# Performance work log

Measured on AMD Instinct MI355X. Metric: run time of the kernel, lower is better.

## Reference

```python
import jax, jax.numpy as jnp
from jax import lax
import numpy as np

D_MODEL = 1024
D_STATE = 16
D_CONV = 4
EXPAND = 2
D_INNER = EXPAND * D_MODEL  # 2048
BATCH = 4
SEQLEN = 2048


def setup_inputs() -> dict:
    key = jax.random.key(0)
    ks = jax.random.split(key, 8)
    s = 0.02  # small init scale for stability
    f32 = jnp.float32
    return {
        "x": jax.random.normal(ks[0], (BATCH, SEQLEN, D_MODEL), f32),
        # Linear weights stored as (in, out); torch applies x @ W.T with W (out, in) -- same math.
        "W_in": (jax.random.normal(ks[1], (D_MODEL, 2 * D_INNER), f32) * s),
        "conv_w": (jax.random.normal(ks[2], (D_INNER, 1, D_CONV), f32) * s),  # depthwise (O, I/groups=1, K)
        "conv_b": jnp.zeros((D_INNER,), f32),
        "W_xproj": (jax.random.normal(ks[3], (D_INNER, 2 * D_STATE), f32) * s),
        "W_dt": (jax.random.normal(ks[4], (D_INNER, D_INNER), f32) * s),
        "b_dt": jnp.zeros((D_INNER,), f32),
        "A_log": jnp.log(jax.random.uniform(ks[5], (D_INNER, D_STATE), f32, 1e-4, 1.0)),
        "D_param": jnp.ones((D_INNER,), f32),
        "W_out": (jax.random.normal(ks[6], (D_INNER, D_MODEL), f32) * s),
    }


def _mamba_forward(x, W_in, conv_w, conv_b, W_xproj, W_dt, b_dt, A_log, D_param, W_out):
    Bb, L, _ = x.shape
    # in_proj and split into x-branch and gate z
    xz = x @ W_in                      # (B, L, 2*d_inner)
    xc, z = jnp.split(xz, 2, axis=-1)
    # causal depthwise conv1d: torch pads both sides by d_conv-1 then slices [:L] == left-pad only
    xt = xc.transpose(0, 2, 1)         # (B, d_inner, L)
    xconv = lax.conv_general_dilated(
        xt, conv_w, window_strides=(1,), padding=[(D_CONV - 1, 0)],
        feature_group_count=D_INNER, dimension_numbers=("NCH", "OIH", "NCH"))
    xs = jax.nn.silu(xconv.transpose(0, 2, 1) + conv_b[None, None, :])  # (B, L, d_inner)
    # SSM inputs
    delta = jax.nn.softplus(xs @ W_dt + b_dt)          # (B, L, d_inner)
    Bs, Cs = jnp.split(xs @ W_xproj, 2, axis=-1)       # each (B, L, d_state)
    A = -jnp.exp(A_log)                                 # (d_inner, d_state)

    def step(h, inp):
        dt, bv, cv, xv = inp                            # (B,d_inner),(B,d_state),(B,d_state),(B,d_inner)
        dA = 1.0 + A[None] * dt[..., None]              # Euler discretization (B, d_inner, d_state)
        dB = bv[:, None, :] * (xv * dt)[..., None]
        h = h * dA + dB
        y = jnp.einsum("bds,bs->bd", h, cv) + D_param * xv
        return h, y

    inputs = (delta.transpose(1, 0, 2), Bs.transpose(1, 0, 2),
              Cs.transpose(1, 0, 2), xs.transpose(1, 0, 2))
    h0 = jnp.zeros((Bb, D_INNER, D_STATE), x.dtype)
    _, ys = lax.scan(step, h0, inputs)                  # ys: (L, B, d_inner)
    y = ys.transpose(1, 0, 2) * jax.nn.silu(z)          # gated output
    return y @ W_out                                    # (B, L, d_model)


def reference(x, W_in, conv_w, conv_b, W_xproj, W_dt, b_dt, A_log, D_param, W_out):
    return _mamba_forward(x, W_in, conv_w, conv_b, W_xproj, W_dt, b_dt, A_log, D_param, W_out)
```

## Files before the change

### kernel.cpp

```cpp
#include <hip/hip_runtime.h>

#define AS1 __attribute__((address_space(1)))
#define AS3 __attribute__((address_space(3)))

typedef unsigned short u16;
typedef unsigned int u32;
typedef __attribute__((ext_vector_type(8))) __bf16 bf16x8;
typedef __attribute__((ext_vector_type(8))) unsigned short u16x8;
typedef __attribute__((ext_vector_type(4))) float f32x4;

#define BATCH   4
#define SEQLEN  2048
#define DMODEL  1024
#define DINNER  2048
#define DSTATE  16
#define ROWS    (BATCH * SEQLEN)

__device__ __forceinline__ u16 f2bf(float f) {
  union { float f; unsigned u; } v; v.f = f;
  unsigned u = v.u;
  return (u16)((u + 0x7fffu + ((u >> 16) & 1u)) >> 16);
}
__device__ __forceinline__ float bf2f(u16 s) {
  union { unsigned u; float f; } v; v.u = ((unsigned)s) << 16;
  return v.f;
}
__device__ __forceinline__ float bflo(u32 p) { union { unsigned u; float f; } v; v.u = p << 16; return v.f; }
__device__ __forceinline__ float bfhi(u32 p) { union { unsigned u; float f; } v; v.u = p & 0xffff0000u; return v.f; }

template<int IMM>
__device__ __forceinline__ bf16x8 dsr(unsigned addr) {
  bf16x8 r;
  asm volatile("ds_read_b128 %0, %1 offset:%2" : "=&v"(r) : "v"(addr), "i"(IMM));
  return r;
}
__device__ __forceinline__ unsigned lds_addr(const u16* p) {
  return (unsigned)(size_t)(const AS3 u16*)p;
}

__global__ void cast_f32_bf16(const float* __restrict__ in, u16* __restrict__ out, int n4) {
  int i = blockIdx.x * blockDim.x + threadIdx.x;
  if (i >= n4) return;
  float4 v = ((const float4*)in)[i];
  ushort4 o;
  o.x = f2bf(v.x); o.y = f2bf(v.y); o.z = f2bf(v.z); o.w = f2bf(v.w);
  ((ushort4*)out)[i] = o;
}

__global__ void transpose_cast(const float* __restrict__ in, u16* __restrict__ out, int R, int C) {
  __shared__ float tile[32][33];
  int x  = blockIdx.x * 32 + threadIdx.x;
  int y0 = blockIdx.y * 32;
#pragma unroll
  for (int j = 0; j < 32; j += 8)
    tile[threadIdx.y + j][threadIdx.x] = in[(size_t)(y0 + threadIdx.y + j) * C + x];
  __syncthreads();
  int xo  = blockIdx.y * 32 + threadIdx.x;
  int yo0 = blockIdx.x * 32;
#pragma unroll
  for (int j = 0; j < 32; j += 8)
    out[(size_t)(yo0 + threadIdx.y + j) * R + xo] = f2bf(tile[threadIdx.x][threadIdx.y + j]);
}

template<int EPI, int BN_>
__launch_bounds__(512, 1)
__global__ void gemm8p(const u16* __restrict__ A, const u16* __restrict__ Bt,
                       void* __restrict__ outp, const float* __restrict__ bias,
                       int M, int N, int K, int gn, int rr, int cc) {
  constexpr int NF   = BN_ / 64;
  constexpr int BCH  = BN_ / 64;
  constexpr int ASZ  = 256 * 64;
  constexpr int BSZ  = BN_ * 64;
  constexpr int BUFS = ASZ + BSZ;
  extern __shared__ u16 lds[];

  const int xcd = blockIdx.x & 7, kb = blockIdx.x >> 3;
  const int tpr = gn / cc;
  const int bm  = (xcd / tpr) * rr + kb / cc;
  const int bn  = (xcd % tpr) * cc + kb % cc;

  const int tid  = threadIdx.x;
  const int wave = tid >> 6, lane = tid & 63;
  const int wm = wave >> 2, wn = wave & 3;
  const int llo = lane & 15, lhi = lane >> 4;
  const size_t bm0 = (size_t)bm * 256, bn0 = (size_t)bn * BN_;
  const int NT = K >> 6;

  const u16* gA[4];
#pragma unroll
  for (int ch = 0; ch < 4; ++ch) {
    int row  = ch * 64 + (tid >> 3);
    int scol = ((tid & 7) ^ (row & 7)) << 3;
    gA[ch] = A + (bm0 + row) * (size_t)K + scol;
  }
  const u16* gB[BCH];
#pragma unroll
  for (int ch = 0; ch < BCH; ++ch) {
    int row  = ch * 64 + (tid >> 3);
    int scol = ((tid & 7) ^ (row & 7)) << 3;
    gB[ch] = Bt + (bn0 + row) * (size_t)K + scol;
  }

  unsigned aA[2][2], aB[2][2];
  {
    const unsigned base0 = lds_addr(lds);
    const unsigned rowA = (unsigned)(wm * 128 + llo) * 128u;
    const unsigned rowB = (unsigned)(wn * (NF * 16) + llo) * 128u;
    const unsigned msk = (unsigned)((llo & 7) << 4);
#pragma unroll
    for (int bf = 0; bf < 2; ++bf)
#pragma unroll
      for (int kk = 0; kk < 2; ++kk) {
        unsigned colk = ((unsigned)(kk * 64 + lhi * 16)) ^ msk;
        aA[bf][kk] = base0 + (unsigned)bf * (BUFS * 2) + rowA + colk;
        aB[bf][kk] = base0 + (unsigned)bf * (BUFS * 2) + (ASZ * 2) + rowB + colk;
      }
  }

#define SGA(t, bsel, ch) __builtin_amdgcn_global_load_lds(                       \
    (const AS1 void*)(gA[ch] + ((size_t)(t) << 6)),                              \
    (AS3 void*)(lds + (bsel) * BUFS + (ch) * 4096 + wave * 512), 16, 0, 0)
#define SGB(t, bsel, ch) __builtin_amdgcn_global_load_lds(                       \
    (const AS1 void*)(gB[ch] + ((size_t)(t) << 6)),                              \
    (AS3 void*)(lds + (bsel) * BUFS + ASZ + (ch) * 4096 + wave * 512), 16, 0, 0)

  f32x4 acc[8][NF] = {};
  bf16x8 bfr[2][4];

#define PHASE(BUF, MH, KK, RDB, STG, WC)                                         \
  {                                                                              \
    bf16x8 af[4];                                                                \
    af[0] = dsr<(MH) * 8192 + 0>(aA[BUF][KK]);                                   \
    af[1] = dsr<(MH) * 8192 + 2048>(aA[BUF][KK]);                                \
    af[2] = dsr<(MH) * 8192 + 4096>(aA[BUF][KK]);                                \
    af[3] = dsr<(MH) * 8192 + 6144>(aA[BUF][KK]);                                \
    if (RDB) {                                                                   \
      bfr[KK][0] = dsr<0>(aB[BUF][KK]);                                          \
      bfr[KK][1] = dsr<2048>(aB[BUF][KK]);                                       \
      if (NF == 4) {                                                             \
        bfr[KK][2] = dsr<4096>(aB[BUF][KK]);                                     \
        bfr[KK][3] = dsr<6144>(aB[BUF][KK]);                                     \
      }                                                                          \
    }                                                                            \
    STG;                                                                         \
    asm volatile("s_barrier" ::: "memory");                                      \
    asm volatile("s_waitcnt lgkmcnt(0)" ::: "memory");                           \
    __builtin_amdgcn_sched_barrier(0);                                           \
    __builtin_amdgcn_s_setprio(1);                                               \
    _Pragma("unroll") for (int m = 0; m < 4; ++m)                                \
      _Pragma("unroll") for (int n = 0; n < NF; ++n)                             \
        acc[(MH) * 4 + m][n] = __builtin_amdgcn_mfma_f32_16x16x32_bf16(          \
            af[m], bfr[KK][n], acc[(MH) * 4 + m][n], 0, 0, 0);                   \
    __builtin_amdgcn_s_setprio(0);                                               \
    WC;                                                                          \
    asm volatile("s_barrier" ::: "memory");                                      \
  }

  SGA(0, 0, 0); SGA(0, 0, 2); SGB(0, 0, 0); SGB(0, 0, 1);
  if (BCH == 4) { SGB(0, 0, 2); SGB(0, 0, 3); }
  SGA(0, 0, 1); SGA(0, 0, 3);
  SGA(1, 1, 0); SGA(1, 1, 2); SGB(1, 1, 0); SGB(1, 1, 1);
  asm volatile("s_waitcnt vmcnt(4)" ::: "memory");
  asm volatile("s_barrier" ::: "memory");

  for (int u = 0; u < NT; u += 2) {
    const int v = u + 1;
    PHASE(0, 0, 0, true,
          ({ if (BCH == 4) { SGB(v, 1, 2); SGB(v, 1, 3); } else { SGA(v, 1, 1); SGA(v, 1, 3); } }),
          ((void)0));
    PHASE(0, 0, 1, true,
          ({ if (BCH == 4) { SGA(v, 1, 1); SGA(v, 1, 3); } }),
          ((void)0));
    PHASE(0, 1, 0, false,
          ({ if (u + 2 < NT) { SGA(u + 2, 0, 0); SGA(u + 2, 0, 2); } }),
          ((void)0));
    PHASE(0, 1, 1, false,
          ({ if (u + 2 < NT) { SGB(u + 2, 0, 0); SGB(u + 2, 0, 1); } }),
          ({ if (u + 2 < NT) asm volatile("s_waitcnt vmcnt(4)" ::: "memory");
             else            asm volatile("s_waitcnt vmcnt(0)" ::: "memory"); }));
    PHASE(1, 0, 0, true,
          ({ if (u + 2 < NT) { if (BCH == 4) { SGB(u + 2, 0, 2); SGB(u + 2, 0, 3); }
                               else          { SGA(u + 2, 0, 1); SGA(u + 2, 0, 3); } } }),
          ((void)0));
    PHASE(1, 0, 1, true,
          ({ if (u + 2 < NT && BCH == 4) { SGA(u + 2, 0, 1); SGA(u + 2, 0, 3); } }),
          ((void)0));
    PHASE(1, 1, 0, false,
          ({ if (v + 2 < NT) { SGA(v + 2, 1, 0); SGA(v + 2, 1, 2); } }),
          ((void)0));
    PHASE(1, 1, 1, false,
          ({ if (v + 2 < NT) { SGB(v + 2, 1, 0); SGB(v + 2, 1, 1); } }),
          ({ if (v + 2 < NT) asm volatile("s_waitcnt vmcnt(4)" ::: "memory");
             else            asm volatile("s_waitcnt vmcnt(0)" ::: "memory"); }));
  }
#undef PHASE
#undef SGA
#undef SGB

#pragma unroll
  for (int am = 0; am < 8; ++am) {
    const int mh = am >> 2, m = am & 3;
    const int rowb = (int)bm0 + wm * 128 + mh * 64 + m * 16 + lhi * 4;
#pragma unroll
    for (int n = 0; n < NF; ++n) {
      const int col = (int)bn0 + wn * (16 * NF) + n * 16 + llo;
#pragma unroll
      for (int r = 0; r < 4; ++r) {
        float v = acc[am][n][r];
        size_t idx = (size_t)(rowb + r) * N + col;
        if (EPI == 0) {
          ((u16*)outp)[idx] = f2bf(v);
        } else if (EPI == 1) {
          float xb = v + bias[col];
          float sp = (xb > 20.f) ? xb : log1pf(__expf(xb));
          ((u16*)outp)[idx] = f2bf(sp);
        } else {
          ((float*)outp)[idx] = v;
        }
      }
    }
  }
}

__global__ void conv_silu4(const u16* __restrict__ xz, const float* __restrict__ w,
                           const float* __restrict__ cb, u16* __restrict__ xs, int total4) {
  int idx = blockIdx.x * 256 + threadIdx.x;
  if (idx >= total4) return;
  int d4 = idx & (DINNER / 4 - 1);
  int l  = (idx >> 9) & (SEQLEN - 1);
  int b  = idx >> 20;
  int d  = d4 * 4;
  float4 wv[4];
#pragma unroll
  for (int j = 0; j < 4; ++j) wv[j] = ((const float4*)w)[d + j];
  float4 bias = *(const float4*)(cb + d);
  float acc[4] = { bias.x, bias.y, bias.z, bias.w };
#pragma unroll
  for (int k = 0; k < 4; ++k) {
    int li = l - 3 + k;
    if (li >= 0) {
      ushort4 xv = *(const ushort4*)(xz + (size_t)(b * SEQLEN + li) * (2 * DINNER) + d);
      acc[0] = fmaf((&wv[0].x)[k], bf2f(xv.x), acc[0]);
      acc[1] = fmaf((&wv[1].x)[k], bf2f(xv.y), acc[1]);
      acc[2] = fmaf((&wv[2].x)[k], bf2f(xv.z), acc[2]);
      acc[3] = fmaf((&wv[3].x)[k], bf2f(xv.w), acc[3]);
    }
  }
  ushort4 o;
  o.x = f2bf(acc[0] / (1.f + __expf(-acc[0])));
  o.y = f2bf(acc[1] / (1.f + __expf(-acc[1])));
  o.z = f2bf(acc[2] / (1.f + __expf(-acc[2])));
  o.w = f2bf(acc[3] / (1.f + __expf(-acc[3])));
  *(ushort4*)(xs + (size_t)idx * 4) = o;
}

__global__ void xproj_kernel(const u16* __restrict__ xs, const float* __restrict__ Wx,
                             float* __restrict__ outp) {
  __shared__ float part[256];
  int row = blockIdx.x;
  int tid = threadIdx.x;
  int c = tid & 31, kp = tid >> 5;
  const u16* xr = xs + (size_t)row * DINNER + kp * 256;
  const float* wp = Wx + (size_t)(kp * 256) * 32 + c;
  float acc = 0.f;
#pragma unroll 4
  for (int kk = 0; kk < 32; ++kk) {
    u16x8 xv = *(const u16x8*)(const void*)(xr + kk * 8);
#pragma unroll
    for (int j = 0; j < 8; ++j)
      acc = fmaf(bf2f(xv[j]), wp[(kk * 8 + j) * 32], acc);
  }
  part[tid] = acc;
  __syncthreads();
  if (tid < 32) {
    float s = 0.f;
#pragma unroll
    for (int p = 0; p < 8; ++p) s += part[p * 32 + tid];
    outp[(size_t)row * 32 + tid] = s;
  }
}

#define SC_NC 32
#define SC_CL 64
#define SC_LDS (2 * SC_NC * 16 * 33 * 4)

__launch_bounds__(512, 1)
__global__ void scan_v3(const u16* __restrict__ delta, const u16* __restrict__ xs,
                        const float* __restrict__ xproj, const u16* __restrict__ xz,
                        const float* __restrict__ A_log, const float* __restrict__ Dp,
                        u16* __restrict__ yg) {
  extern __shared__ float smem[];
  float* cP = smem;
  float* cH = smem + SC_NC * 16 * 33;
  const int tid = threadIdx.x;
  const int dl = tid & 15, ck = tid >> 4;
  const int b = blockIdx.x >> 6, dblk = blockIdx.x & 63;
  const int d0 = dblk * 32 + dl * 2;
  const int r0 = b * SEQLEN + ck * SC_CL;

  float A0[DSTATE], A1[DSTATE];
  {
    const f32x4* ap0 = (const f32x4*)(A_log + (size_t)d0 * DSTATE);
    const f32x4* ap1 = (const f32x4*)(A_log + (size_t)(d0 + 1) * DSTATE);
#pragma unroll
    for (int q = 0; q < 4; ++q) {
      f32x4 a0 = ap0[q], a1 = ap1[q];
#pragma unroll
      for (int j = 0; j < 4; ++j) { A0[q * 4 + j] = -__expf(a0[j]); A1[q * 4 + j] = -__expf(a1[j]); }
    }
  }

  const u32* dP = (const u32*)(delta + (size_t)r0 * DINNER + d0);
  const u32* xP = (const u32*)(xs    + (size_t)r0 * DINNER + d0);
  const u32* zP = (const u32*)(xz + (size_t)r0 * (2 * DINNER) + DINNER + d0);
  const float* bP = xproj + (size_t)r0 * 32;
  const int DW = DINNER / 2;
  const int ZW = DINNER;

  float P0[DSTATE], P1[DSTATE], H0[DSTATE], H1[DSTATE];
#pragma unroll
  for (int s = 0; s < DSTATE; ++s) { P0[s] = P1[s] = 1.f; H0[s] = H1[s] = 0.f; }
  {
    u32 dq0 = dP[0], xq0 = xP[0];
    u32 dq1 = dP[DW], xq1 = xP[DW];
    f32x4 Bn[4];
#pragma unroll
    for (int q = 0; q < 4; ++q) Bn[q] = ((const f32x4*)bP)[q];
    for (int l = 0; l < SC_CL; ++l) {
      const u32 dc = dq0, xc = xq0;
      dq0 = dq1; xq0 = xq1;
      if (l + 2 < SC_CL) { dq1 = dP[(l + 2) * DW]; xq1 = xP[(l + 2) * DW]; }
      f32x4 Bc[4] = { Bn[0], Bn[1], Bn[2], Bn[3] };
      if (l + 1 < SC_CL) {
        const f32x4* bn = (const f32x4*)(bP + (l + 1) * 32);
#pragma unroll
        for (int q = 0; q < 4; ++q) Bn[q] = bn[q];
      }
      float dt0 = bflo(dc), dt1 = bfhi(dc);
      float x0 = bflo(xc),  x1 = bfhi(xc);
      float dtx0 = dt0 * x0, dtx1 = dt1 * x1;
#pragma unroll
      for (int s = 0; s < DSTATE; ++s) {
        float bs = Bc[s >> 2][s & 3];
        float dA0 = fmaf(A0[s], dt0, 1.f);
        float dA1 = fmaf(A1[s], dt1, 1.f);
        P0[s] *= dA0; P1[s] *= dA1;
        H0[s] = fmaf(H0[s], dA0, bs * dtx0);
        H1[s] = fmaf(H1[s], dA1, bs * dtx1);
      }
    }
  }
  {
    float* p = cP + (ck * 16 + dl) * 33;
    float* h = cH + (ck * 16 + dl) * 33;
#pragma unroll
    for (int s = 0; s < DSTATE; ++s) {
      p[s] = P0[s]; p[16 + s] = P1[s];
      h[s] = H0[s]; h[16 + s] = H1[s];
    }
  }
  __syncthreads();

  {
    const int s2 = tid & 15, dd = tid >> 4;
    const int idx = (dd & 1) * 16 + s2;
    float* pbase = cP + (dd >> 1) * 33 + idx;
    float* hbase = cH + (dd >> 1) * 33 + idx;
    float h = 0.f;
    for (int c = 0; c < SC_NC; ++c) {
      float p = pbase[c * 16 * 33], hh = hbase[c * 16 * 33];
      pbase[c * 16 * 33] = h;
      h = fmaf(p, h, hh);
    }
  }
  __syncthreads();

  float h0[DSTATE], h1[DSTATE];
  {
    const float* p = cP + (ck * 16 + dl) * 33;
#pragma unroll
    for (int s = 0; s < DSTATE; ++s) { h0[s] = p[s]; h1[s] = p[16 + s]; }
  }
  const float Dv0 = Dp[d0], Dv1 = Dp[d0 + 1];
  u32* yP = (u32*)(yg + (size_t)r0 * DINNER + d0);
  {
    u32 dq0 = dP[0], xq0 = xP[0], zq0 = zP[0];
    u32 dq1 = dP[DW], xq1 = xP[DW], zq1 = zP[ZW];
    f32x4 Bn[4], Cn[4];
#pragma unroll
    for (int q = 0; q < 4; ++q) { Bn[q] = ((const f32x4*)bP)[q]; Cn[q] = ((const f32x4*)bP)[q + 4]; }
    for (int l = 0; l < SC_CL; ++l) {
      const u32 dc = dq0, xc = xq0, zc = zq0;
      dq0 = dq1; xq0 = xq1; zq0 = zq1;
      if (l + 2 < SC_CL) { dq1 = dP[(l + 2) * DW]; xq1 = xP[(l + 2) * DW]; zq1 = zP[(l + 2) * ZW]; }
      f32x4 Bc[4] = { Bn[0], Bn[1], Bn[2], Bn[3] };
      f32x4 Cc[4] = { Cn[0], Cn[1], Cn[2], Cn[3] };
      if (l + 1 < SC_CL) {
        const f32x4* bn = (const f32x4*)(bP + (l + 1) * 32);
#pragma unroll
        for (int q = 0; q < 4; ++q) { Bn[q] = bn[q]; Cn[q] = bn[q + 4]; }
      }
      float dt0 = bflo(dc), dt1 = bfhi(dc);
      float x0 = bflo(xc),  x1 = bfhi(xc);
      float dtx0 = dt0 * x0, dtx1 = dt1 * x1;
      float yp0 = 0.f, yp1 = 0.f;
#pragma unroll
      for (int s = 0; s < DSTATE; ++s) {
        float bs = Bc[s >> 2][s & 3];
        float cs = Cc[s >> 2][s & 3];
        float dA0 = fmaf(A0[s], dt0, 1.f);
        float dA1 = fmaf(A1[s], dt1, 1.f);
        h0[s] = fmaf(h0[s], dA0, bs * dtx0);
        h1[s] = fmaf(h1[s], dA1, bs * dtx1);
        yp0 = fmaf(h0[s], cs, yp0);
        yp1 = fmaf(h1[s], cs, yp1);
      }
      float z0 = bflo(zc), z1 = bfhi(zc);
      float y0 = (yp0 + Dv0 * x0) * (z0 / (1.f + __expf(-z0)));
      float y1 = (yp1 + Dv1 * x1) * (z1 / (1.f + __expf(-z1)));
      yP[l * DW] = (u32)f2bf(y0) | ((u32)f2bf(y1) << 16);
    }
  }
}

extern "C" void kernel_launch(void* const* d_in, const int* in_sizes, int n_in,
                              void* d_out, int out_size, void* d_ws, size_t ws_size,
                              hipStream_t stream) {
  const float* x       = (const float*)d_in[0];
  const float* W_in    = (const float*)d_in[1];
  const float* conv_w  = (const float*)d_in[2];
  const float* conv_b  = (const float*)d_in[3];
  const float* W_xproj = (const float*)d_in[4];
  const float* W_dt    = (const float*)d_in[5];
  const float* b_dt    = (const float*)d_in[6];
  const float* A_log   = (const float*)d_in[7];
  const float* D_param = (const float*)d_in[8];
  const float* W_out   = (const float*)d_in[9];
  float* out = (float*)d_out;

  char* ws = (char*)d_ws;
  const size_t MB = 1ull << 20;
  u16*   x_bf  = (u16*)(ws);
  u16*   WinT  = (u16*)(ws + 16 * MB);
  u16*   WdtT  = (u16*)(ws + 24 * MB);
  u16*   xz_bf = (u16*)(ws + 32 * MB);
  u16*   xs_bf = (u16*)(ws + 96 * MB);
  u16*   delta = (u16*)(ws + 128 * MB);
  float* xpj   = (float*)(ws + 192 * MB);
  u16*   WoutT = (u16*)(ws + 193 * MB);
  u16*   yg    = (u16*)(ws);

  hipFuncSetAttribute((const void*)gemm8p<0, 256>, hipFuncAttributeMaxDynamicSharedMemorySize, 131072);
  hipFuncSetAttribute((const void*)gemm8p<1, 256>, hipFuncAttributeMaxDynamicSharedMemorySize, 131072);
  hipFuncSetAttribute((const void*)gemm8p<2, 128>, hipFuncAttributeMaxDynamicSharedMemorySize, 98304);
  hipFuncSetAttribute((const void*)scan_v3, hipFuncAttributeMaxDynamicSharedMemorySize, SC_LDS);

  dim3 tb(32, 8);

  cast_f32_bf16<<<(ROWS * DMODEL / 4 + 255) / 256, 256, 0, stream>>>(x, x_bf, ROWS * DMODEL / 4);
  transpose_cast<<<dim3((2 * DINNER) / 32, DMODEL / 32), tb, 0, stream>>>(W_in, WinT, DMODEL, 2 * DINNER);
  transpose_cast<<<dim3(DINNER / 32, DINNER / 32), tb, 0, stream>>>(W_dt, WdtT, DINNER, DINNER);
  transpose_cast<<<dim3(DMODEL / 32, DINNER / 32), tb, 0, stream>>>(W_out, WoutT, DINNER, DMODEL);

  gemm8p<0, 256><<<512, 512, 131072, stream>>>(x_bf, WinT, xz_bf, nullptr,
                                               ROWS, 2 * DINNER, DMODEL, 16, 8, 8);

  conv_silu4<<<(ROWS * DINNER / 4) / 256, 256, 0, stream>>>(
      xz_bf, conv_w, conv_b, xs_bf, ROWS * DINNER / 4);

  gemm8p<1, 256><<<256, 512, 131072, stream>>>(xs_bf, WdtT, delta, b_dt,
                                               ROWS, DINNER, DINNER, 8, 4, 8);

  xproj_kernel<<<ROWS, 256, 0, stream>>>(xs_bf, W_xproj, xpj);

  scan_v3<<<BATCH * (DINNER / 32), 512, SC_LDS, stream>>>(
      delta, xs_bf, xpj, xz_bf, A_log, D_param, yg);

  gemm8p<2, 128><<<256, 512, 98304, stream>>>(yg, WoutT, out, nullptr,
                                              ROWS, DMODEL, DINNER, 8, 4, 8);
}
```

Measured before the change: 473.6 us.

## Software-pipeline LDS fragment reads with double-buffered A registers in GEMM loop

Restructures the GEMM main loop so the LDS reads for the next MFMA phase are issued before the current phase's MFMAs, using two A-fragment register sets and partial lgkmcnt waits instead of a full wait. It also reorders the global-to-LDS staging schedule and prologue and removes one barrier per phase. The aim is to hide LDS read latency behind matrix-core work. In exchange it raises register pressure and makes the wait counts and barrier placement more fragile, which could cause races if any count is off.

```diff
diff --git a/kernel.cpp b/kernel.cpp
--- a/kernel.cpp
+++ b/kernel.cpp
@@ -36,6 +36,11 @@
 }
 __device__ __forceinline__ unsigned lds_addr(const u16* p) {
   return (unsigned)(size_t)(const AS3 u16*)p;
+}
+template<int N>
+__device__ __forceinline__ void lgkm() {
+  asm volatile("s_waitcnt lgkmcnt(%0)" :: "i"(N) : "memory");
+  __builtin_amdgcn_sched_barrier(0);
 }
 
 __global__ void cast_f32_bf16(const float* __restrict__ in, u16* __restrict__ out, int n4) {
@@ -125,75 +130,81 @@
     (AS3 void*)(lds + (bsel) * BUFS + ASZ + (ch) * 4096 + wave * 512), 16, 0, 0)
 
   f32x4 acc[8][NF] = {};
+  bf16x8 af[2][4];
   bf16x8 bfr[2][4];
 
-#define PHASE(BUF, MH, KK, RDB, STG, WC)                                         \
-  {                                                                              \
-    bf16x8 af[4];                                                                \
-    af[0] = dsr<(MH) * 8192 + 0>(aA[BUF][KK]);                                   \
-    af[1] = dsr<(MH) * 8192 + 2048>(aA[BUF][KK]);                                \
-    af[2] = dsr<(MH) * 8192 + 4096>(aA[BUF][KK]);                                \
-    af[3] = dsr<(MH) * 8192 + 6144>(aA[BUF][KK]);                                \
-    if (RDB) {                                                                   \
-      bfr[KK][0] = dsr<0>(aB[BUF][KK]);                                          \
-      bfr[KK][1] = dsr<2048>(aB[BUF][KK]);                                       \
-      if (NF == 4) {                                                             \
-        bfr[KK][2] = dsr<4096>(aB[BUF][KK]);                                     \
-        bfr[KK][3] = dsr<6144>(aB[BUF][KK]);                                     \
-      }                                                                          \
+#define RD_A(SET, BF, KK, MH) do {                                               \
+    af[SET][0] = dsr<(MH) * 8192 + 0>(aA[BF][KK]);                               \
+    af[SET][1] = dsr<(MH) * 8192 + 2048>(aA[BF][KK]);                            \
+    af[SET][2] = dsr<(MH) * 8192 + 4096>(aA[BF][KK]);                            \
+    af[SET][3] = dsr<(MH) * 8192 + 6144>(aA[BF][KK]);                            \
+  } while (0)
+#define RD_B(BF, KK) do {                                                        \
+    bfr[KK][0] = dsr<0>(aB[BF][KK]);                                             \
+    bfr[KK][1] = dsr<2048>(aB[BF][KK]);                                          \
+    if constexpr (NF == 4) {                                                     \
+      bfr[KK][2] = dsr<4096>(aB[BF][KK]);                                        \
+      bfr[KK][3] = dsr<6144>(aB[BF][KK]);                                        \
     }                                                                            \
-    STG;                                                                         \
-    asm volatile("s_barrier" ::: "memory");                                      \
-    asm volatile("s_waitcnt lgkmcnt(0)" ::: "memory");                           \
-    __builtin_amdgcn_sched_barrier(0);                                           \
+  } while (0)
+#define MM(SET, KK, MH) do {                                                     \
     __builtin_amdgcn_s_setprio(1);                                               \
     _Pragma("unroll") for (int m = 0; m < 4; ++m)                                \
       _Pragma("unroll") for (int n = 0; n < NF; ++n)                             \
         acc[(MH) * 4 + m][n] = __builtin_amdgcn_mfma_f32_16x16x32_bf16(          \
-            af[m], bfr[KK][n], acc[(MH) * 4 + m][n], 0, 0, 0);                   \
+            af[SET][m], bfr[KK][n], acc[(MH) * 4 + m][n], 0, 0, 0);              \
     __builtin_amdgcn_s_setprio(0);                                               \
-    WC;                                                                          \
-    asm volatile("s_barrier" ::: "memory");                                      \
-  }
-
-  SGA(0, 0, 0); SGA(0, 0, 2); SGB(0, 0, 0); SGB(0, 0, 1);
-  if (BCH == 4) { SGB(0, 0, 2); SGB(0, 0, 3); }
-  SGA(0, 0, 1); SGA(0, 0, 3);
-  SGA(1, 1, 0); SGA(1, 1, 2); SGB(1, 1, 0); SGB(1, 1, 1);
-  asm volatile("s_waitcnt vmcnt(4)" ::: "memory");
-  asm volatile("s_barrier" ::: "memory");
+  } while (0)
+#define BAR asm volatile("s_barrier" ::: "memory")
+
+  SGA(0, 0, 0); SGA(0, 0, 2); SGA(0, 0, 1); SGA(0, 0, 3);
+  SGB(0, 0, 0); SGB(0, 0, 1);
+  if constexpr (BCH == 4) { SGB(0, 0, 2); SGB(0, 0, 3); }
+  SGB(1, 1, 0); SGB(1, 1, 1);
+  if constexpr (BCH == 4) { SGB(1, 1, 2); SGB(1, 1, 3); }
+  if constexpr (BCH == 4) asm volatile("s_waitcnt vmcnt(4)" ::: "memory");
+  else                    asm volatile("s_waitcnt vmcnt(2)" ::: "memory");
+  BAR;
+  RD_A(0, 0, 0, 0); RD_B(0, 0);
 
   for (int u = 0; u < NT; u += 2) {
-    const int v = u + 1;
-    PHASE(0, 0, 0, true,
-          ({ if (BCH == 4) { SGB(v, 1, 2); SGB(v, 1, 3); } else { SGA(v, 1, 1); SGA(v, 1, 3); } }),
-          ((void)0));
-    PHASE(0, 0, 1, true,
-          ({ if (BCH == 4) { SGA(v, 1, 1); SGA(v, 1, 3); } }),
-          ((void)0));
-    PHASE(0, 1, 0, false,
-          ({ if (u + 2 < NT) { SGA(u + 2, 0, 0); SGA(u + 2, 0, 2); } }),
-          ((void)0));
-    PHASE(0, 1, 1, false,
-          ({ if (u + 2 < NT) { SGB(u + 2, 0, 0); SGB(u + 2, 0, 1); } }),
-          ({ if (u + 2 < NT) asm volatile("s_waitcnt vmcnt(4)" ::: "memory");
-             else            asm volatile("s_waitcnt vmcnt(0)" ::: "memory"); }));
-    PHASE(1, 0, 0, true,
-          ({ if (u + 2 < NT) { if (BCH == 4) { SGB(u + 2, 0, 2); SGB(u + 2, 0, 3); }
-                               else          { SGA(u + 2, 0, 1); SGA(u + 2, 0, 3); } } }),
-          ((void)0));
-    PHASE(1, 0, 1, true,
-          ({ if (u + 2 < NT && BCH == 4) { SGA(u + 2, 0, 1); SGA(u + 2, 0, 3); } }),
-          ((void)0));
-    PHASE(1, 1, 0, false,
-          ({ if (v + 2 < NT) { SGA(v + 2, 1, 0); SGA(v + 2, 1, 2); } }),
-          ((void)0));
-    PHASE(1, 1, 1, false,
-          ({ if (v + 2 < NT) { SGB(v + 2, 1, 0); SGB(v + 2, 1, 1); } }),
-          ({ if (v + 2 < NT) asm volatile("s_waitcnt vmcnt(4)" ::: "memory");
-             else            asm volatile("s_waitcnt vmcnt(0)" ::: "memory"); }));
-  }
-#undef PHASE
+    const bool c2 = (u + 2) < NT, c3 = (u + 3) < NT;
+    RD_A(1, 0, 1, 0); RD_B(0, 1);
+    SGA(u + 1, 1, 0); SGA(u + 1, 1, 2);
+    lgkm<4 + NF>(); MM(0, 0, 0); BAR;
+    RD_A(0, 0, 0, 1);
+    SGA(u + 1, 1, 1); SGA(u + 1, 1, 3);
+    lgkm<4>(); MM(1, 1, 0); BAR;
+    RD_A(1, 0, 1, 1);
+    if (c2) { SGB(u + 2, 0, 0); SGB(u + 2, 0, 1); }
+    lgkm<4>(); MM(0, 0, 1);
+    if (c2) asm volatile("s_waitcnt vmcnt(2)" ::: "memory");
+    else    asm volatile("s_waitcnt vmcnt(0)" ::: "memory");
+    BAR;
+    RD_A(0, 1, 0, 0); RD_B(1, 0);
+    if (c2) { if constexpr (BCH == 4) { SGB(u + 2, 0, 2); SGB(u + 2, 0, 3); } }
+    lgkm<4 + NF>(); MM(1, 1, 1); BAR;
+    RD_A(1, 1, 1, 0); RD_B(1, 1);
+    if (c2) { SGA(u + 2, 0, 0); SGA(u + 2, 0, 2); }
+    lgkm<4 + NF>(); MM(0, 0, 0); BAR;
+    RD_A(0, 1, 0, 1);
+    if (c2) { SGA(u + 2, 0, 1); SGA(u + 2, 0, 3); }
+    lgkm<4>(); MM(1, 1, 0); BAR;
+    RD_A(1, 1, 1, 1);
+    if (c3) { SGB(u + 3, 1, 0); SGB(u + 3, 1, 1); }
+    lgkm<4>(); MM(0, 0, 1);
+    if (c3) asm volatile("s_waitcnt vmcnt(2)" ::: "memory");
+    else    asm volatile("s_waitcnt vmcnt(0)" ::: "memory");
+    BAR;
+    RD_A(0, 0, 0, 0); RD_B(0, 0);
+    if (c3) { if constexpr (BCH == 4) { SGB(u + 3, 1, 2); SGB(u + 3, 1, 3); } }
+    lgkm<4 + NF>(); MM(1, 1, 1); BAR;
+  }
+  asm volatile("s_waitcnt vmcnt(0) lgkmcnt(0)" ::: "memory");
+#undef RD_A
+#undef RD_B
+#undef MM
+#undef BAR
 #undef SGA
 #undef SGB
 
```

Measured after the change: 541.3 us. +14.3%, slower.

## Split chunked scan into carry, compose, and emit kernels with global carries

Applied to the files above, without the earlier changes.

The single fused scan kernel, which used LDS and block-wide syncs to combine per-chunk carries, is split into three kernels. scan_carry computes per-chunk products and states and writes them to global workspace. scan_compose does the sequential prefix over chunks, and scan_emit recomputes outputs from the composed initial states. The goal is more blocks at smaller size (256 threads, 3 per CU) for better occupancy and no LDS. The cost is extra launches and global traffic for the carries (about 16 MB each way).

```diff
diff --git a/kernel.cpp b/kernel.cpp
--- a/kernel.cpp
+++ b/kernel.cpp
@@ -280,21 +280,17 @@
   }
 }
 
-#define SC_NC 32
 #define SC_CL 64
-#define SC_LDS (2 * SC_NC * 16 * 33 * 4)
-
-__launch_bounds__(512, 1)
-__global__ void scan_v3(const u16* __restrict__ delta, const u16* __restrict__ xs,
-                        const float* __restrict__ xproj, const u16* __restrict__ xz,
-                        const float* __restrict__ A_log, const float* __restrict__ Dp,
-                        u16* __restrict__ yg) {
-  extern __shared__ float smem[];
-  float* cP = smem;
-  float* cH = smem + SC_NC * 16 * 33;
+
+__launch_bounds__(256, 3)
+__global__ void scan_carry(const u16* __restrict__ delta, const u16* __restrict__ xs,
+                           const float* __restrict__ xproj, const float* __restrict__ A_log,
+                           float* __restrict__ Pg, float* __restrict__ Hg) {
   const int tid = threadIdx.x;
-  const int dl = tid & 15, ck = tid >> 4;
-  const int b = blockIdx.x >> 6, dblk = blockIdx.x & 63;
+  const int dl = tid & 15, ckl = tid >> 4;
+  const int b = blockIdx.x >> 7;
+  const int dblk = (blockIdx.x >> 1) & 63;
+  const int ck = (blockIdx.x & 1) * 16 + ckl;
   const int d0 = dblk * 32 + dl * 2;
   const int r0 = b * SEQLEN + ck * SC_CL;
 
@@ -312,10 +308,8 @@
 
   const u32* dP = (const u32*)(delta + (size_t)r0 * DINNER + d0);
   const u32* xP = (const u32*)(xs    + (size_t)r0 * DINNER + d0);
-  const u32* zP = (const u32*)(xz + (size_t)r0 * (2 * DINNER) + DINNER + d0);
   const float* bP = xproj + (size_t)r0 * 32;
   const int DW = DINNER / 2;
-  const int ZW = DINNER;
 
   float P0[DSTATE], P1[DSTATE], H0[DSTATE], H1[DSTATE];
 #pragma unroll
@@ -350,37 +344,80 @@
       }
     }
   }
+  const size_t base = ((size_t)(b * 32 + ck) * DINNER + d0) * DSTATE;
+  f32x4* Pp = (f32x4*)(Pg + base);
+  f32x4* Hp = (f32x4*)(Hg + base);
+#pragma unroll
+  for (int q = 0; q < 4; ++q) {
+    f32x4 p0 = { P0[4 * q], P0[4 * q + 1], P0[4 * q + 2], P0[4 * q + 3] };
+    f32x4 p1 = { P1[4 * q], P1[4 * q + 1], P1[4 * q + 2], P1[4 * q + 3] };
+    f32x4 h0 = { H0[4 * q], H0[4 * q + 1], H0[4 * q + 2], H0[4 * q + 3] };
+    f32x4 h1 = { H1[4 * q], H1[4 * q + 1], H1[4 * q + 2], H1[4 * q + 3] };
+    Pp[q] = p0; Pp[4 + q] = p1;
+    Hp[q] = h0; Hp[4 + q] = h1;
+  }
+}
+
+__global__ void scan_compose(float* __restrict__ Pg, const float* __restrict__ Hg) {
+  const int gid = blockIdx.x * 256 + threadIdx.x;
+  const int s = gid & 15;
+  const int d = (gid >> 4) & (DINNER - 1);
+  const int b = gid >> 15;
+  const size_t cstride = (size_t)DINNER * DSTATE;
+  size_t idx = ((size_t)(b * 32) * DINNER + d) * DSTATE + s;
+  float h = 0.f;
+#pragma unroll 4
+  for (int c = 0; c < 32; ++c) {
+    float p = Pg[idx], hh = Hg[idx];
+    Pg[idx] = h;
+    h = fmaf(p, h, hh);
+    idx += cstride;
+  }
+}
+
+__launch_bounds__(256, 3)
+__global__ void scan_emit(const u16* __restrict__ delta, const u16* __restrict__ xs,
+                          const float* __restrict__ xproj, const u16* __restrict__ xz,
+                          const float* __restrict__ A_log, const float* __restrict__ Dp,
+                          const float* __restrict__ Pg, u16* __restrict__ yg) {
+  const int tid = threadIdx.x;
+  const int dl = tid & 15, ckl = tid >> 4;
+  const int b = blockIdx.x >> 7;
+  const int dblk = (blockIdx.x >> 1) & 63;
+  const int ck = (blockIdx.x & 1) * 16 + ckl;
+  const int d0 = dblk * 32 + dl * 2;
+  const int r0 = b * SEQLEN + ck * SC_CL;
+
+  float A0[DSTATE], A1[DSTATE];
   {
-    float* p = cP + (ck * 16 + dl) * 33;
-    float* h = cH + (ck * 16 + dl) * 33;
-#pragma unroll
-    for (int s = 0; s < DSTATE; ++s) {
-      p[s] = P0[s]; p[16 + s] = P1[s];
-      h[s] = H0[s]; h[16 + s] = H1[s];
-    }
-  }
-  __syncthreads();
-
-  {
-    const int s2 = tid & 15, dd = tid >> 4;
-    const int idx = (dd & 1) * 16 + s2;
-    float* pbase = cP + (dd >> 1) * 33 + idx;
-    float* hbase = cH + (dd >> 1) * 33 + idx;
-    float h = 0.f;
-    for (int c = 0; c < SC_NC; ++c) {
-      float p = pbase[c * 16 * 33], hh = hbase[c * 16 * 33];
-      pbase[c * 16 * 33] = h;
-      h = fmaf(p, h, hh);
-    }
-  }
-  __syncthreads();
+    const f32x4* ap0 = (const f32x4*)(A_log + (size_t)d0 * DSTATE);
+    const f32x4* ap1 = (const f32x4*)(A_log + (size_t)(d0 + 1) * DSTATE);
+#pragma unroll
+    for (int q = 0; q < 4; ++q) {
+      f32x4 a0 = ap0[q], a1 = ap1[q];
+#pragma unroll
+      for (int j = 0; j < 4; ++j) { A0[q * 4 + j] = -__expf(a0[j]); A1[q * 4 + j] = -__expf(a1[j]); }
+    }
+  }
 
   float h0[DSTATE], h1[DSTATE];
   {
-    const float* p = cP + (ck * 16 + dl) * 33;
-#pragma unroll
-    for (int s = 0; s < DSTATE; ++s) { h0[s] = p[s]; h1[s] = p[16 + s]; }
-  }
+    const size_t base = ((size_t)(b * 32 + ck) * DINNER + d0) * DSTATE;
+    const f32x4* Pp = (const f32x4*)(Pg + base);
+#pragma unroll
+    for (int q = 0; q < 4; ++q) {
+      f32x4 v0 = Pp[q], v1 = Pp[4 + q];
+#pragma unroll
+      for (int j = 0; j < 4; ++j) { h0[4 * q + j] = v0[j]; h1[4 * q + j] = v1[j]; }
+    }
+  }
+
+  const u32* dP = (const u32*)(delta + (size_t)r0 * DINNER + d0);
+  const u32* xP = (const u32*)(xs    + (size_t)r0 * DINNER + d0);
+  const u32* zP = (const u32*)(xz + (size_t)r0 * (2 * DINNER) + DINNER + d0);
+  const float* bP = xproj + (size_t)r0 * 32;
+  const int DW = DINNER / 2;
+  const int ZW = DINNER;
   const float Dv0 = Dp[d0], Dv1 = Dp[d0 + 1];
   u32* yP = (u32*)(yg + (size_t)r0 * DINNER + d0);
   {
@@ -446,14 +483,15 @@
   u16*   xz_bf = (u16*)(ws + 32 * MB);
   u16*   xs_bf = (u16*)(ws + 96 * MB);
   u16*   delta = (u16*)(ws + 128 * MB);
+  float* Pg    = (float*)(ws + 160 * MB);
   float* xpj   = (float*)(ws + 192 * MB);
   u16*   WoutT = (u16*)(ws + 193 * MB);
+  float* Hg    = (float*)(ws);
   u16*   yg    = (u16*)(ws);
 
   hipFuncSetAttribute((const void*)gemm8p<0, 256>, hipFuncAttributeMaxDynamicSharedMemorySize, 131072);
   hipFuncSetAttribute((const void*)gemm8p<1, 256>, hipFuncAttributeMaxDynamicSharedMemorySize, 131072);
   hipFuncSetAttribute((const void*)gemm8p<2, 128>, hipFuncAttributeMaxDynamicSharedMemorySize, 98304);
-  hipFuncSetAttribute((const void*)scan_v3, hipFuncAttributeMaxDynamicSharedMemorySize, SC_LDS);
 
   dim3 tb(32, 8);
 
@@ -473,8 +511,9 @@
 
   xproj_kernel<<<ROWS, 256, 0, stream>>>(xs_bf, W_xproj, xpj);
 
-  scan_v3<<<BATCH * (DINNER / 32), 512, SC_LDS, stream>>>(
-      delta, xs_bf, xpj, xz_bf, A_log, D_param, yg);
+  scan_carry<<<512, 256, 0, stream>>>(delta, xs_bf, xpj, A_log, Pg, Hg);
+  scan_compose<<<512, 256, 0, stream>>>(Pg, Hg);
+  scan_emit<<<512, 256, 0, stream>>>(delta, xs_bf, xpj, xz_bf, A_log, D_param, Pg, yg);
 
   gemm8p<2, 128><<<256, 512, 98304, stream>>>(yg, WoutT, out, nullptr,
                                               ROWS, DMODEL, DINNER, 8, 4, 8);
```

Measured after the change: 503.3 us (median of 2 runs). 1.06x slower.

## Replace 8-phase GEMM pipeline with simpler double-buffered per-K-tile schedule

Applied to the files above, without the earlier changes.

Replaces the fine-grained eight-phase ping-pong GEMM main loop, which interleaved partial LDS reads, global-to-LDS staging and two barriers per phase, with a per-K-tile loop. Each tile issues all staging loads for the next buffer, reads all A/B fragments for both K halves, waits on lgkmcnt in two steps to overlap the second half's reads with the first half's MFMAs, then waits vmcnt(0) and barriers once. This cuts barrier count and scheduling complexity but holds more fragment registers and exposes a full vmcnt(0) wait each tile, which may reduce latency hiding of global loads.

```diff
diff --git a/kernel.cpp b/kernel.cpp
--- a/kernel.cpp
+++ b/kernel.cpp
@@ -36,6 +36,11 @@
 }
 __device__ __forceinline__ unsigned lds_addr(const u16* p) {
   return (unsigned)(size_t)(const AS3 u16*)p;
+}
+template<int N>
+__device__ __forceinline__ void lgkm() {
+  asm volatile("s_waitcnt lgkmcnt(%0)" :: "i"(N) : "memory");
+  __builtin_amdgcn_sched_barrier(0);
 }
 
 __global__ void cast_f32_bf16(const float* __restrict__ in, u16* __restrict__ out, int n4) {
@@ -125,75 +130,61 @@
     (AS3 void*)(lds + (bsel) * BUFS + ASZ + (ch) * 4096 + wave * 512), 16, 0, 0)
 
   f32x4 acc[8][NF] = {};
-  bf16x8 bfr[2][4];
-
-#define PHASE(BUF, MH, KK, RDB, STG, WC)                                         \
+
+#define MM(AV, BV)                                                               \
+    __builtin_amdgcn_s_setprio(1);                                               \
+    _Pragma("unroll") for (int mh = 0; mh < 2; ++mh)                             \
+      _Pragma("unroll") for (int m = 0; m < 4; ++m)                              \
+        _Pragma("unroll") for (int n = 0; n < NF; ++n)                           \
+          acc[mh * 4 + m][n] = __builtin_amdgcn_mfma_f32_16x16x32_bf16(          \
+              AV[mh * 4 + m], BV[n], acc[mh * 4 + m][n], 0, 0, 0);               \
+    __builtin_amdgcn_s_setprio(0);
+
+#define KTILE(BUF, DOSTG, TNEXT)                                                 \
   {                                                                              \
-    bf16x8 af[4];                                                                \
-    af[0] = dsr<(MH) * 8192 + 0>(aA[BUF][KK]);                                   \
-    af[1] = dsr<(MH) * 8192 + 2048>(aA[BUF][KK]);                                \
-    af[2] = dsr<(MH) * 8192 + 4096>(aA[BUF][KK]);                                \
-    af[3] = dsr<(MH) * 8192 + 6144>(aA[BUF][KK]);                                \
-    if (RDB) {                                                                   \
-      bfr[KK][0] = dsr<0>(aB[BUF][KK]);                                          \
-      bfr[KK][1] = dsr<2048>(aB[BUF][KK]);                                       \
-      if (NF == 4) {                                                             \
-        bfr[KK][2] = dsr<4096>(aB[BUF][KK]);                                     \
-        bfr[KK][3] = dsr<6144>(aB[BUF][KK]);                                     \
-      }                                                                          \
+    if (DOSTG) {                                                                 \
+      SGA(TNEXT, (BUF) ^ 1, 0); SGA(TNEXT, (BUF) ^ 1, 1);                        \
+      SGA(TNEXT, (BUF) ^ 1, 2); SGA(TNEXT, (BUF) ^ 1, 3);                        \
+      SGB(TNEXT, (BUF) ^ 1, 0); SGB(TNEXT, (BUF) ^ 1, 1);                        \
+      if (BCH == 4) { SGB(TNEXT, (BUF) ^ 1, 2); SGB(TNEXT, (BUF) ^ 1, 3); }      \
     }                                                                            \
-    STG;                                                                         \
+    bf16x8 a0[8], a1[8], b0[NF], b1[NF];                                         \
+    a0[0] = dsr<0>(aA[BUF][0]);     a0[1] = dsr<2048>(aA[BUF][0]);               \
+    a0[2] = dsr<4096>(aA[BUF][0]);  a0[3] = dsr<6144>(aA[BUF][0]);               \
+    a0[4] = dsr<8192>(aA[BUF][0]);  a0[5] = dsr<10240>(aA[BUF][0]);              \
+    a0[6] = dsr<12288>(aA[BUF][0]); a0[7] = dsr<14336>(aA[BUF][0]);              \
+    b0[0] = dsr<0>(aB[BUF][0]);     b0[1] = dsr<2048>(aB[BUF][0]);               \
+    if constexpr (NF == 4) {                                                     \
+      b0[2] = dsr<4096>(aB[BUF][0]); b0[3] = dsr<6144>(aB[BUF][0]);              \
+    }                                                                            \
+    a1[0] = dsr<0>(aA[BUF][1]);     a1[1] = dsr<2048>(aA[BUF][1]);               \
+    a1[2] = dsr<4096>(aA[BUF][1]);  a1[3] = dsr<6144>(aA[BUF][1]);               \
+    a1[4] = dsr<8192>(aA[BUF][1]);  a1[5] = dsr<10240>(aA[BUF][1]);              \
+    a1[6] = dsr<12288>(aA[BUF][1]); a1[7] = dsr<14336>(aA[BUF][1]);              \
+    b1[0] = dsr<0>(aB[BUF][1]);     b1[1] = dsr<2048>(aB[BUF][1]);               \
+    if constexpr (NF == 4) {                                                     \
+      b1[2] = dsr<4096>(aB[BUF][1]); b1[3] = dsr<6144>(aB[BUF][1]);              \
+    }                                                                            \
+    lgkm<8 + NF>();                 \
+    MM(a0, b0);                                                                  \
+    lgkm<0>();                                                                   \
+    MM(a1, b1);                                                                  \
+    asm volatile("s_waitcnt vmcnt(0)" ::: "memory");                             \
     asm volatile("s_barrier" ::: "memory");                                      \
-    asm volatile("s_waitcnt lgkmcnt(0)" ::: "memory");                           \
-    __builtin_amdgcn_sched_barrier(0);                                           \
-    __builtin_amdgcn_s_setprio(1);                                               \
-    _Pragma("unroll") for (int m = 0; m < 4; ++m)                                \
-      _Pragma("unroll") for (int n = 0; n < NF; ++n)                             \
-        acc[(MH) * 4 + m][n] = __builtin_amdgcn_mfma_f32_16x16x32_bf16(          \
-            af[m], bfr[KK][n], acc[(MH) * 4 + m][n], 0, 0, 0);                   \
-    __builtin_amdgcn_s_setprio(0);                                               \
-    WC;                                                                          \
-    asm volatile("s_barrier" ::: "memory");                                      \
-  }
-
-  SGA(0, 0, 0); SGA(0, 0, 2); SGB(0, 0, 0); SGB(0, 0, 1);
+  }
+
+  SGA(0, 0, 0); SGA(0, 0, 1); SGA(0, 0, 2); SGA(0, 0, 3);
+  SGB(0, 0, 0); SGB(0, 0, 1);
   if (BCH == 4) { SGB(0, 0, 2); SGB(0, 0, 3); }
-  SGA(0, 0, 1); SGA(0, 0, 3);
-  SGA(1, 1, 0); SGA(1, 1, 2); SGB(1, 1, 0); SGB(1, 1, 1);
-  asm volatile("s_waitcnt vmcnt(4)" ::: "memory");
+  asm volatile("s_waitcnt vmcnt(0)" ::: "memory");
   asm volatile("s_barrier" ::: "memory");
 
   for (int u = 0; u < NT; u += 2) {
-    const int v = u + 1;
-    PHASE(0, 0, 0, true,
-          ({ if (BCH == 4) { SGB(v, 1, 2); SGB(v, 1, 3); } else { SGA(v, 1, 1); SGA(v, 1, 3); } }),
-          ((void)0));
-    PHASE(0, 0, 1, true,
-          ({ if (BCH == 4) { SGA(v, 1, 1); SGA(v, 1, 3); } }),
-          ((void)0));
-    PHASE(0, 1, 0, false,
-          ({ if (u + 2 < NT) { SGA(u + 2, 0, 0); SGA(u + 2, 0, 2); } }),
-          ((void)0));
-    PHASE(0, 1, 1, false,
-          ({ if (u + 2 < NT) { SGB(u + 2, 0, 0); SGB(u + 2, 0, 1); } }),
-          ({ if (u + 2 < NT) asm volatile("s_waitcnt vmcnt(4)" ::: "memory");
-             else            asm volatile("s_waitcnt vmcnt(0)" ::: "memory"); }));
-    PHASE(1, 0, 0, true,
-          ({ if (u + 2 < NT) { if (BCH == 4) { SGB(u + 2, 0, 2); SGB(u + 2, 0, 3); }
-                               else          { SGA(u + 2, 0, 1); SGA(u + 2, 0, 3); } } }),
-          ((void)0));
-    PHASE(1, 0, 1, true,
-          ({ if (u + 2 < NT && BCH == 4) { SGA(u + 2, 0, 1); SGA(u + 2, 0, 3); } }),
-          ((void)0));
-    PHASE(1, 1, 0, false,
-          ({ if (v + 2 < NT) { SGA(v + 2, 1, 0); SGA(v + 2, 1, 2); } }),
-          ((void)0));
-    PHASE(1, 1, 1, false,
-          ({ if (v + 2 < NT) { SGB(v + 2, 1, 0); SGB(v + 2, 1, 1); } }),
-          ({ if (v + 2 < NT) asm volatile("s_waitcnt vmcnt(4)" ::: "memory");
-             else            asm volatile("s_waitcnt vmcnt(0)" ::: "memory"); }));
-  }
-#undef PHASE
+    KTILE(0, true, u + 1);
+    KTILE(1, (u + 2) < NT, u + 2);
+  }
+#undef KTILE
+#undef MM
 #undef SGA
 #undef SGB
 
```

After: 598.8 us. +26.5%, slower.
